# Kernel optimization log

Hardware: AMD Instinct MI355X
Metric: run time of the kernel (lower is better)

## Reference

```python
import jax, jax.numpy as jnp
import numpy as np

B, S, D, P = 8, 2048, 512, 64  # batch, seq, num_embed_hidden, num_attention_project


def setup_inputs() -> dict:
    key = jax.random.key(0)
    ks = jax.random.split(key, 9)
    sd = 1.0 / np.sqrt(D)
    sp = 1.0 / np.sqrt(P)
    return {
        "query": jax.random.normal(ks[0], (B, S, D), dtype=jnp.float32),
        "attention_mask": jnp.ones((B, S), dtype=jnp.float32),
        "Wq": jax.random.uniform(ks[1], (D, P), jnp.float32, -sd, sd),
        "bq": jax.random.uniform(ks[2], (P,), jnp.float32, -sd, sd),
        "Wk": jax.random.uniform(ks[3], (D, P), jnp.float32, -sd, sd),
        "bk": jax.random.uniform(ks[4], (P,), jnp.float32, -sd, sd),
        "Wv": jax.random.uniform(ks[5], (D, P), jnp.float32, -sd, sd),
        "bv": jax.random.uniform(ks[6], (P,), jnp.float32, -sd, sd),
        "Wo": jax.random.uniform(ks[7], (P, D), jnp.float32, -sp, sp),
        "bo": jax.random.uniform(ks[8], (D,), jnp.float32, -sp, sp),
    }


def reference(query, attention_mask, Wq, bq, Wk, bk, Wv, bv, Wo, bo):
    q = jnp.einsum("bsd,dp->bsp", query, Wq) + bq  # [B,S,P]
    k = jnp.einsum("bsd,dp->bsp", query, Wk) + bk
    v = jnp.einsum("bsd,dp->bsp", query, Wv) + bv
    scores = jnp.einsum("bsp,btp->bst", q, k) / jnp.sqrt(jnp.float32(P))  # [B,S,S]
    # Faithful to original: mask broadcast over last axis via unsqueeze(-1) -> masks rows
    scores = scores + (1.0 - attention_mask[:, :, None]) * -10000.0
    weights = jax.nn.softmax(scores, axis=-1)
    weighted = jnp.einsum("bst,btp->bsp", weights, v)
    return jnp.einsum("bsp,pd->bsd", weighted, Wo) + bo
```

## Files before the change

kernel.cpp:

```cpp
#include <hip/hip_runtime.h>
#include <hip/hip_bf16.h>
#include <math.h>

constexpr int B = 8;
constexpr int S = 2048;
constexpr int D = 512;
constexpr int P = 64;
constexpr float SCALE = 0.125f;

typedef short bf16x8 __attribute__((ext_vector_type(8)));
typedef float f32x4 __attribute__((ext_vector_type(4)));
typedef unsigned int u32;

__device__ __forceinline__ unsigned short f2bf(float x) {
  __hip_bfloat16 h = __float2bfloat16(x);
  return __builtin_bit_cast(unsigned short, h);
}
__device__ __forceinline__ float bf2f(unsigned short u) {
  unsigned int v = (unsigned int)u << 16;
  return __builtin_bit_cast(float, v);
}


__global__ __launch_bounds__(256) void prep_w(
    const float* __restrict__ Wq, const float* __restrict__ Wk,
    const float* __restrict__ Wv, const float* __restrict__ Wo,
    unsigned short* __restrict__ Bfrag, unsigned short* __restrict__ Wofrag) {
  const int i = blockIdx.x * 256 + threadIdx.x;
  if (i < 192 * 512) {
    const int d = i / 192;
    const int n = i - d * 192;
    const float* W = (n < 64) ? Wq : (n < 128) ? Wk : Wv;
    const float val = W[d * 64 + (n & 63)];
    const int nt = n >> 4, l15 = n & 15;
    const int k16 = d >> 5, l4 = (d >> 3) & 3, j = d & 7;
    Bfrag[(((nt * 16 + k16) * 4 + l4) * 16 + l15) * 8 + j] = f2bf(val);
  }
  if (i < 64 * 512) {
    const int k = i >> 9;
    const int n = i & 511;
    const float val = Wo[k * 512 + n];
    const int ct = n >> 4, l15 = n & 15;
    const int h = k >> 5, l4 = (k >> 3) & 3, j = k & 7;
    Wofrag[(((ct * 2 + h) * 4 + l4) * 16 + l15) * 8 + j] = f2bf(val);
  }
}

__global__ __launch_bounds__(256, 4) void qkv_mfma(
    const float* __restrict__ query, const unsigned short* __restrict__ Bfrag,
    const float* __restrict__ bq, const float* __restrict__ bk,
    const float* __restrict__ bv, unsigned short* __restrict__ qfrag,
    unsigned short* __restrict__ kfrag, unsigned short* __restrict__ vfrag) {
  __shared__ __align__(16) unsigned short Aq[16 * 512];

  const int tid = threadIdx.x;
  const int w = tid >> 6;
  const int l = tid & 63;
  const int l15 = l & 15;
  const int l4 = l >> 4;
  const int s0 = blockIdx.x * 16;
  const int kb0 = blockIdx.x & 15;

  const float* qsrc = query + (size_t)s0 * D;
#pragma unroll
  for (int step = 0; step < 4; ++step) {
    const int row = step * 4 + w;
    const float* pf = qsrc + row * D + l * 8;
    const float4 x = *(const float4*)pf;
    const float4 y = *(const float4*)(pf + 4);
    bf16x8 u;
    u[0] = (short)f2bf(x.x); u[1] = (short)f2bf(x.y);
    u[2] = (short)f2bf(x.z); u[3] = (short)f2bf(x.w);
    u[4] = (short)f2bf(y.x); u[5] = (short)f2bf(y.y);
    u[6] = (short)f2bf(y.z); u[7] = (short)f2bf(y.w);
    *(bf16x8*)&Aq[row * 512 + ((l ^ (row & 7)) << 3)] = u;
  }
  __syncthreads();

  f32x4 acc[3];
#pragma unroll
  for (int nt = 0; nt < 3; ++nt) acc[nt] = (f32x4){0.f, 0.f, 0.f, 0.f};

#pragma unroll
  for (int kk = 0; kk < 16; ++kk) {
    const int k16 = (kk + kb0) & 15;
    const int aslot = (k16 * 4 + l4) ^ (l15 & 7);
    const bf16x8 af = *(const bf16x8*)&Aq[l15 * 512 + (aslot << 3)];
#pragma unroll
    for (int nt = 0; nt < 3; ++nt) {
      const int ntg = w * 3 + nt;
      const bf16x8 bf =
          *(const bf16x8*)(Bfrag + ((size_t)(ntg * 16 + k16) * 64 + l) * 8);
      acc[nt] = __builtin_amdgcn_mfma_f32_16x16x32_bf16(af, bf, acc[nt], 0, 0,
                                                        0);
    }
  }

  const int b = s0 >> 11;
  const size_t bbase = (size_t)b * (S * P);
#pragma unroll
  for (int nt = 0; nt < 3; ++nt) {
    const int col = w * 48 + nt * 16 + l15;
    const int mat = col >> 6;
    const int p = col & 63;
    const float bb = ((mat == 0) ? bq : (mat == 1) ? bk : bv)[p];
#pragma unroll
    for (int r = 0; r < 4; ++r) {
      const int s = s0 + l4 * 4 + r;
      const int t = s & 2047;
      const float vl = acc[nt][r] + bb;
      if (mat == 2) {
        const int tb = t >> 5, chv = (t >> 3) & 3, jv = t & 7;
        const int pcv = p >> 4, rowv = p & 15;
        vfrag[bbase + (((size_t)(tb * 4 + pcv) * 4 + chv) * 16 + rowv) * 8 +
              jv] = f2bf(vl);
      } else {
        const int tile = t >> 4, rowin = t & 15;
        const int h = p >> 5, chp = (p >> 3) & 3, j = p & 7;
        unsigned short* dst = (mat == 0) ? qfrag : kfrag;
        dst[bbase + (((size_t)(tile * 2 + h) * 4 + chp) * 16 + rowin) * 8 +
            j] = f2bf(mat == 0 ? vl * SCALE : vl);
      }
    }
  }
}

__global__ __launch_bounds__(1024, 4) void attn_fused(
    const unsigned short* __restrict__ qfrag,
    const unsigned short* __restrict__ kfrag,
    const unsigned short* __restrict__ vfrag,
    const unsigned short* __restrict__ Wofrag, const float* __restrict__ bo,
    float* __restrict__ out) {
  __shared__ __align__(16) unsigned char smem[131072];
  __shared__ float l_s[16][32];

  const int tid = threadIdx.x;
  const int w = tid >> 6;
  const int lane = tid & 63;
  const int l15 = lane & 15;
  const int l4 = lane >> 4;
  const int qg = w & 1;
  const int th = w >> 1;

  const int blk = blockIdx.x;
  const int b = blk & 7;
  const int qt = blk >> 3;
  const int s0 = qt * 64;
  const int wst = qt & 3;

  const size_t bbase = (size_t)b * (S * P);
  const unsigned short* qf = qfrag + bbase;
  const unsigned short* kf = kfrag + bbase;
  const unsigned short* vf = vfrag + bbase;

  unsigned short* e_w = (unsigned short*)smem + w * 4096;

  bf16x8 aq[2][2];
#pragma unroll
  for (int st = 0; st < 2; ++st)
#pragma unroll
    for (int h = 0; h < 2; ++h)
      aq[st][h] =
          *(const bf16x8*)(qf +
                           ((size_t)(((s0 >> 4) + qg * 2 + st) * 2 + h) * 64 +
                            lane) *
                               8);

  f32x4 acc[2][4];
#pragma unroll
  for (int st = 0; st < 2; ++st)
#pragma unroll
    for (int pc = 0; pc < 4; ++pc) acc[st][pc] = (f32x4){0.f, 0.f, 0.f, 0.f};
  float lpart[2][4] = {{0.f, 0.f, 0.f, 0.f}, {0.f, 0.f, 0.f, 0.f}};

  for (int win = 0; win < 4; ++win) {
    const int wi = (win + wst) & 3;
    const int t0 = th * 256 + wi * 64;
    unsigned short* e_s = e_w + (win & 1) * 2048;

    bf16x8 bk[4][2];
#pragma unroll
    for (int nt = 0; nt < 4; ++nt)
#pragma unroll
      for (int h = 0; h < 2; ++h)
        bk[nt][h] =
            *(const bf16x8*)(kf +
                             ((size_t)(((t0 >> 4) + nt) * 2 + h) * 64 + lane) *
                                 8);

#pragma unroll
    for (int st = 0; st < 2; ++st) {
      f32x4 sc[4];
#pragma unroll
      for (int nt = 0; nt < 4; ++nt) {
        f32x4 c = (f32x4){0.f, 0.f, 0.f, 0.f};
        c = __builtin_amdgcn_mfma_f32_16x16x32_bf16(aq[st][0], bk[nt][0], c, 0,
                                                    0, 0);
        sc[nt] = __builtin_amdgcn_mfma_f32_16x16x32_bf16(aq[st][1], bk[nt][1],
                                                         c, 0, 0, 0);
      }
#pragma unroll
      for (int nt = 0; nt < 4; ++nt) {
        const int ch = nt * 2 + (l15 >> 3);
#pragma unroll
        for (int r = 0; r < 4; ++r) {
          const int rr = l4 * 4 + r;
          const unsigned short eu = f2bf(__expf(sc[nt][r]));
          lpart[st][r] += bf2f(eu);
          e_s[st * 1024 + rr * 64 + ((ch ^ (rr & 7)) << 3) + (l15 & 7)] = eu;
        }
      }
    }

    bf16x8 bv[4][2];
#pragma unroll
    for (int pc = 0; pc < 4; ++pc)
#pragma unroll
      for (int kk = 0; kk < 2; ++kk)
        bv[pc][kk] =
            *(const bf16x8*)(vf +
                             ((size_t)(((t0 >> 5) + kk) * 4 + pc) * 64 + lane) *
                                 8);

#pragma unroll
    for (int st = 0; st < 2; ++st) {
      bf16x8 ae[2];
#pragma unroll
      for (int kk = 0; kk < 2; ++kk)
        ae[kk] = *(const bf16x8*)&e_s[st * 1024 + l15 * 64 +
                                      (((kk * 4 + l4) ^ (l15 & 7)) << 3)];
#pragma unroll
      for (int pc = 0; pc < 4; ++pc) {
        acc[st][pc] = __builtin_amdgcn_mfma_f32_16x16x32_bf16(
            ae[0], bv[pc][0], acc[st][pc], 0, 0, 0);
        acc[st][pc] = __builtin_amdgcn_mfma_f32_16x16x32_bf16(
            ae[1], bv[pc][1], acc[st][pc], 0, 0, 0);
      }
    }
  }

#pragma unroll
  for (int st = 0; st < 2; ++st)
#pragma unroll
    for (int r = 0; r < 4; ++r) {
      float v = lpart[st][r];
      v += __shfl_xor(v, 1, 64);
      v += __shfl_xor(v, 2, 64);
      v += __shfl_xor(v, 4, 64);
      v += __shfl_xor(v, 8, 64);
      if (l15 == 0) l_s[w][st * 16 + l4 * 4 + r] = v;
    }

  __syncthreads();

  float* pacc = (float*)smem;
  if (th > 0) {
#pragma unroll
    for (int st = 0; st < 2; ++st)
#pragma unroll
      for (int pc = 0; pc < 4; ++pc)
#pragma unroll
        for (int r = 0; r < 4; ++r)
          pacc[((size_t)(qg * 7 + th - 1) * 32 + st * 16 + l4 * 4 + r) * 64 +
               pc * 16 + l15] = acc[st][pc][r];
  }
  __syncthreads();

  unsigned short* wnorm = (unsigned short*)(smem + 114688);
  if (th == 0) {
#pragma unroll
    for (int st = 0; st < 2; ++st) {
      float rl[4];
#pragma unroll
      for (int r = 0; r < 4; ++r) {
        const int row = st * 16 + l4 * 4 + r;
        float ls = 0.f;
#pragma unroll
        for (int t8 = 0; t8 < 8; ++t8) ls += l_s[t8 * 2 + qg][row];
        rl[r] = 1.f / ls;
      }
#pragma unroll
      for (int pc = 0; pc < 4; ++pc)
#pragma unroll
        for (int r = 0; r < 4; ++r) {
          float s = acc[st][pc][r];
#pragma unroll
          for (int j = 0; j < 7; ++j)
            s += pacc[((size_t)(qg * 7 + j) * 32 + st * 16 + l4 * 4 + r) * 64 +
                      pc * 16 + l15];
          wnorm[(qg * 32 + st * 16 + l4 * 4 + r) * 64 + pc * 16 + l15] =
              f2bf(s * rl[r]);
        }
    }
  }
  __syncthreads();

  const int sub = w & 3;
  const int chq = w >> 2;
  const bf16x8 a0 = *(const bf16x8*)&wnorm[(sub * 16 + l15) * 64 + l4 * 8];
  const bf16x8 a1 =
      *(const bf16x8*)&wnorm[(sub * 16 + l15) * 64 + 32 + l4 * 8];
  const size_t orow0 = (size_t)b * S + s0 + sub * 16;
#pragma unroll
  for (int ct = 0; ct < 8; ++ct) {
    const int ctg = chq * 8 + ((ct + (blk & 7)) & 7);
    const bf16x8 b0 =
        *(const bf16x8*)(Wofrag + ((size_t)(ctg * 2 + 0) * 64 + lane) * 8);
    const bf16x8 b1 =
        *(const bf16x8*)(Wofrag + ((size_t)(ctg * 2 + 1) * 64 + lane) * 8);
    f32x4 c = (f32x4){0.f, 0.f, 0.f, 0.f};
    c = __builtin_amdgcn_mfma_f32_16x16x32_bf16(a0, b0, c, 0, 0, 0);
    c = __builtin_amdgcn_mfma_f32_16x16x32_bf16(a1, b1, c, 0, 0, 0);
    const int col = ctg * 16 + l15;
    const float bb = bo[col];
#pragma unroll
    for (int r = 0; r < 4; ++r)
      out[(orow0 + l4 * 4 + r) * D + col] = c[r] + bb;
  }
}

extern "C" void kernel_launch(void* const* d_in, const int* in_sizes, int n_in,
                              void* d_out, int out_size, void* d_ws,
                              size_t ws_size, hipStream_t stream) {
  const float* query = (const float*)d_in[0];
  const float* Wq = (const float*)d_in[2];
  const float* bq = (const float*)d_in[3];
  const float* Wk = (const float*)d_in[4];
  const float* bk = (const float*)d_in[5];
  const float* Wv = (const float*)d_in[6];
  const float* bv = (const float*)d_in[7];
  const float* Wo = (const float*)d_in[8];
  const float* bo = (const float*)d_in[9];
  float* out = (float*)d_out;

  const size_t proj = (size_t)B * S * P;
  unsigned short* qfr = (unsigned short*)d_ws;
  unsigned short* kfr = qfr + proj;
  unsigned short* vfr = kfr + proj;
  unsigned short* Bfrag = vfr + proj;
  unsigned short* Wofrag = Bfrag + 192 * 512;

  prep_w<<<384, 256, 0, stream>>>(Wq, Wk, Wv, Wo, Bfrag, Wofrag);
  qkv_mfma<<<1024, 256, 0, stream>>>(query, Bfrag, bq, bk, bv, qfr, kfr, vfr);
  attn_fused<<<256, 1024, 0, stream>>>(qfr, kfr, vfr, Wofrag, bo, out);
}
```

Before: 139.9 us.

## Stage K/V and weight tiles into LDS via async global-to-LDS loads with double buffering

The QKV projection now processes 64 rows per block with 512 threads. Its weight fragments are staged into double-buffered LDS through global_load_lds, so eight waves share each weight load. The attention kernel handles 128 query rows per block and stages K/V tiles cooperatively into double-buffered LDS, so waves no longer each fetch K/V from global memory. The intent is to cut redundant global/L2 traffic. The cost is half as many blocks (128 attention blocks on a large GPU), which lowers parallelism, plus a barrier per iteration.

```diff
diff --git a/kernel.cpp b/kernel.cpp
--- a/kernel.cpp
+++ b/kernel.cpp
@@ -19,6 +19,13 @@
 __device__ __forceinline__ float bf2f(unsigned short u) {
   unsigned int v = (unsigned int)u << 16;
   return __builtin_bit_cast(float, v);
+}
+
+__device__ __forceinline__ void ld_g2lds16(const unsigned short* g,
+                                           unsigned short* l) {
+  __builtin_amdgcn_global_load_lds(
+      (const __attribute__((address_space(1))) u32*)g,
+      (__attribute__((address_space(3))) u32*)l, 16, 0, 0);
 }
 
 
@@ -46,25 +53,28 @@
   }
 }
 
-__global__ __launch_bounds__(256, 4) void qkv_mfma(
+__global__ __launch_bounds__(512, 2) void qkv_mfma(
     const float* __restrict__ query, const unsigned short* __restrict__ Bfrag,
     const float* __restrict__ bq, const float* __restrict__ bk,
     const float* __restrict__ bv, unsigned short* __restrict__ qfrag,
     unsigned short* __restrict__ kfrag, unsigned short* __restrict__ vfrag) {
-  __shared__ __align__(16) unsigned short Aq[16 * 512];
+  __shared__ __align__(16) unsigned short Aq[64 * 512];
+  __shared__ __align__(16) unsigned short Bb[2][24 * 512];
 
   const int tid = threadIdx.x;
   const int w = tid >> 6;
   const int l = tid & 63;
   const int l15 = l & 15;
   const int l4 = l >> 4;
-  const int s0 = blockIdx.x * 16;
-  const int kb0 = blockIdx.x & 15;
+  const int s0 = blockIdx.x * 64;
+  const int rg = w & 3;
+  const int ch = w >> 2;
+  const int phase = blockIdx.x & 7;
 
   const float* qsrc = query + (size_t)s0 * D;
 #pragma unroll
-  for (int step = 0; step < 4; ++step) {
-    const int row = step * 4 + w;
+  for (int step = 0; step < 8; ++step) {
+    const int row = step * 8 + w;
     const float* pf = qsrc + row * D + l * 8;
     const float4 x = *(const float4*)pf;
     const float4 y = *(const float4*)(pf + 4);
@@ -75,40 +85,58 @@
     u[6] = (short)f2bf(y.z); u[7] = (short)f2bf(y.w);
     *(bf16x8*)&Aq[row * 512 + ((l ^ (row & 7)) << 3)] = u;
   }
+
+#define STAGE_B(kc, buf)                                                      \
+  {                                                                           \
+    _Pragma("unroll") for (int i = 0; i < 3; ++i) {                           \
+      const int cid = w * 3 + i;                                              \
+      const int nt = cid >> 1, kb = cid & 1;                                  \
+      const unsigned short* gp =                                              \
+          Bfrag + (size_t)(nt * 16 + (kc)*2 + kb) * 512 + (size_t)l * 8;      \
+      ld_g2lds16(gp, &Bb[buf][cid * 512]);                                    \
+    }                                                                         \
+  }
+
+  STAGE_B(phase, 0);
   __syncthreads();
 
-  f32x4 acc[3];
-#pragma unroll
-  for (int nt = 0; nt < 3; ++nt) acc[nt] = (f32x4){0.f, 0.f, 0.f, 0.f};
-
-#pragma unroll
-  for (int kk = 0; kk < 16; ++kk) {
-    const int k16 = (kk + kb0) & 15;
-    const int aslot = (k16 * 4 + l4) ^ (l15 & 7);
-    const bf16x8 af = *(const bf16x8*)&Aq[l15 * 512 + (aslot << 3)];
-#pragma unroll
-    for (int nt = 0; nt < 3; ++nt) {
-      const int ntg = w * 3 + nt;
-      const bf16x8 bf =
-          *(const bf16x8*)(Bfrag + ((size_t)(ntg * 16 + k16) * 64 + l) * 8);
-      acc[nt] = __builtin_amdgcn_mfma_f32_16x16x32_bf16(af, bf, acc[nt], 0, 0,
-                                                        0);
-    }
+  f32x4 acc[6];
+#pragma unroll
+  for (int j = 0; j < 6; ++j) acc[j] = (f32x4){0.f, 0.f, 0.f, 0.f};
+
+  for (int it = 0; it < 8; ++it) {
+    const int kc = (it + phase) & 7;
+    if (it < 7) STAGE_B((it + 1 + phase) & 7, (it + 1) & 1);
+    const unsigned short* Bcur = &Bb[it & 1][0];
+#pragma unroll
+    for (int kb = 0; kb < 2; ++kb) {
+      const int row = rg * 16 + l15;
+      const int slot = ((kc * 2 + kb) * 4 + l4) ^ (row & 7);
+      const bf16x8 af = *(const bf16x8*)&Aq[row * 512 + (slot << 3)];
+#pragma unroll
+      for (int j = 0; j < 6; ++j) {
+        const bf16x8 bfr =
+            *(const bf16x8*)&Bcur[((ch * 6 + j) * 2 + kb) * 512 + l * 8];
+        acc[j] =
+            __builtin_amdgcn_mfma_f32_16x16x32_bf16(af, bfr, acc[j], 0, 0, 0);
+      }
+    }
+    __syncthreads();
   }
 
   const int b = s0 >> 11;
   const size_t bbase = (size_t)b * (S * P);
 #pragma unroll
-  for (int nt = 0; nt < 3; ++nt) {
-    const int col = w * 48 + nt * 16 + l15;
+  for (int j = 0; j < 6; ++j) {
+    const int col = ch * 96 + j * 16 + l15;
     const int mat = col >> 6;
     const int p = col & 63;
     const float bb = ((mat == 0) ? bq : (mat == 1) ? bk : bv)[p];
 #pragma unroll
     for (int r = 0; r < 4; ++r) {
-      const int s = s0 + l4 * 4 + r;
+      const int s = s0 + rg * 16 + l4 * 4 + r;
       const int t = s & 2047;
-      const float vl = acc[nt][r] + bb;
+      const float vl = acc[j][r] + bb;
       if (mat == 2) {
         const int tb = t >> 5, chv = (t >> 3) & 3, jv = t & 7;
         const int pcv = p >> 4, rowv = p & 15;
@@ -116,13 +144,14 @@
               jv] = f2bf(vl);
       } else {
         const int tile = t >> 4, rowin = t & 15;
-        const int h = p >> 5, chp = (p >> 3) & 3, j = p & 7;
+        const int h = p >> 5, chp = (p >> 3) & 3, jj = p & 7;
         unsigned short* dst = (mat == 0) ? qfrag : kfrag;
         dst[bbase + (((size_t)(tile * 2 + h) * 4 + chp) * 16 + rowin) * 8 +
-            j] = f2bf(mat == 0 ? vl * SCALE : vl);
-      }
-    }
-  }
+            jj] = f2bf(mat == 0 ? vl * SCALE : vl);
+      }
+    }
+  }
+#undef STAGE_B
 }
 
 __global__ __launch_bounds__(1024, 4) void attn_fused(
@@ -131,7 +160,7 @@
     const unsigned short* __restrict__ vfrag,
     const unsigned short* __restrict__ Wofrag, const float* __restrict__ bo,
     float* __restrict__ out) {
-  __shared__ __align__(16) unsigned char smem[131072];
+  __shared__ __align__(16) unsigned char smem[116736];
   __shared__ float l_s[16][32];
 
   const int tid = threadIdx.x;
@@ -139,21 +168,22 @@
   const int lane = tid & 63;
   const int l15 = lane & 15;
   const int l4 = lane >> 4;
-  const int qg = w & 1;
-  const int th = w >> 1;
+  const int qg = w & 3;
+  const int th = w >> 2;
 
   const int blk = blockIdx.x;
   const int b = blk & 7;
-  const int qt = blk >> 3;
-  const int s0 = qt * 64;
-  const int wst = qt & 3;
+  const int s0 = (blk >> 3) * 128;
+  const int phase = (blk >> 3) & 15;
 
   const size_t bbase = (size_t)b * (S * P);
   const unsigned short* qf = qfrag + bbase;
   const unsigned short* kf = kfrag + bbase;
   const unsigned short* vf = vfrag + bbase;
 
-  unsigned short* e_w = (unsigned short*)smem + w * 4096;
+  unsigned short* kb0 = (unsigned short*)smem;
+  unsigned short* vb0 = (unsigned short*)(smem + 32768);
+  unsigned short* e_w = (unsigned short*)(smem + 65536) + w * 1024;
 
   bf16x8 aq[2][2];
 #pragma unroll
@@ -173,26 +203,43 @@
     for (int pc = 0; pc < 4; ++pc) acc[st][pc] = (f32x4){0.f, 0.f, 0.f, 0.f};
   float lpart[2][4] = {{0.f, 0.f, 0.f, 0.f}, {0.f, 0.f, 0.f, 0.f}};
 
-  for (int win = 0; win < 4; ++win) {
-    const int wi = (win + wst) & 3;
-    const int t0 = th * 256 + wi * 64;
-    unsigned short* e_s = e_w + (win & 1) * 2048;
-
-    bf16x8 bk[4][2];
-#pragma unroll
-    for (int nt = 0; nt < 4; ++nt)
+#define STAGE_KV(wi, buf)                                                     \
+  {                                                                           \
+    const int t0s = (wi)*128;                                                 \
+    const unsigned short* gpk =                                               \
+        kf + ((size_t)((t0s >> 4) + (w >> 1)) * 2 + (w & 1)) * 512 +          \
+        (size_t)lane * 8;                                                     \
+    ld_g2lds16(gpk, kb0 + (buf)*8192 + w * 512);                              \
+    const unsigned short* gpv =                                               \
+        vf + ((size_t)((t0s >> 5) + (w >> 2)) * 4 + (w & 3)) * 512 +          \
+        (size_t)lane * 8;                                                     \
+    ld_g2lds16(gpv, vb0 + (buf)*8192 + w * 512);                              \
+  }
+
+  STAGE_KV(phase, 0);
+  __syncthreads();
+
+  for (int it = 0; it < 16; ++it) {
+    if (it < 15) STAGE_KV((it + 1 + phase) & 15, (it + 1) & 1);
+    const unsigned short* kt = kb0 + (it & 1) * 8192 + th * 2048;
+    const unsigned short* vt = vb0 + (it & 1) * 8192 + th * 2048;
+
+    bf16x8 bk[2][2];
+#pragma unroll
+    for (int nt = 0; nt < 2; ++nt)
 #pragma unroll
       for (int h = 0; h < 2; ++h)
-        bk[nt][h] =
-            *(const bf16x8*)(kf +
-                             ((size_t)(((t0 >> 4) + nt) * 2 + h) * 64 + lane) *
-                                 8);
+        bk[nt][h] = *(const bf16x8*)&kt[nt * 1024 + h * 512 + lane * 8];
+    bf16x8 bv[4];
+#pragma unroll
+    for (int pc = 0; pc < 4; ++pc)
+      bv[pc] = *(const bf16x8*)&vt[pc * 512 + lane * 8];
 
 #pragma unroll
     for (int st = 0; st < 2; ++st) {
-      f32x4 sc[4];
-#pragma unroll
-      for (int nt = 0; nt < 4; ++nt) {
+      f32x4 sc[2];
+#pragma unroll
+      for (int nt = 0; nt < 2; ++nt) {
         f32x4 c = (f32x4){0.f, 0.f, 0.f, 0.f};
         c = __builtin_amdgcn_mfma_f32_16x16x32_bf16(aq[st][0], bk[nt][0], c, 0,
                                                     0, 0);
@@ -200,44 +247,27 @@
                                                          c, 0, 0, 0);
       }
 #pragma unroll
-      for (int nt = 0; nt < 4; ++nt) {
-        const int ch = nt * 2 + (l15 >> 3);
+      for (int nt = 0; nt < 2; ++nt) {
+        const int chl = nt * 2 + (l15 >> 3);
 #pragma unroll
         for (int r = 0; r < 4; ++r) {
           const int rr = l4 * 4 + r;
           const unsigned short eu = f2bf(__expf(sc[nt][r]));
           lpart[st][r] += bf2f(eu);
-          e_s[st * 1024 + rr * 64 + ((ch ^ (rr & 7)) << 3) + (l15 & 7)] = eu;
+          e_w[st * 512 + rr * 32 + ((chl ^ (rr & 3)) << 3) + (l15 & 7)] = eu;
         }
       }
-    }
-
-    bf16x8 bv[4][2];
-#pragma unroll
-    for (int pc = 0; pc < 4; ++pc)
-#pragma unroll
-      for (int kk = 0; kk < 2; ++kk)
-        bv[pc][kk] =
-            *(const bf16x8*)(vf +
-                             ((size_t)(((t0 >> 5) + kk) * 4 + pc) * 64 + lane) *
-                                 8);
-
-#pragma unroll
-    for (int st = 0; st < 2; ++st) {
-      bf16x8 ae[2];
-#pragma unroll
-      for (int kk = 0; kk < 2; ++kk)
-        ae[kk] = *(const bf16x8*)&e_s[st * 1024 + l15 * 64 +
-                                      (((kk * 4 + l4) ^ (l15 & 7)) << 3)];
-#pragma unroll
-      for (int pc = 0; pc < 4; ++pc) {
-        acc[st][pc] = __builtin_amdgcn_mfma_f32_16x16x32_bf16(
-            ae[0], bv[pc][0], acc[st][pc], 0, 0, 0);
-        acc[st][pc] = __builtin_amdgcn_mfma_f32_16x16x32_bf16(
-            ae[1], bv[pc][1], acc[st][pc], 0, 0, 0);
-      }
-    }
-  }
+      const bf16x8 ae =
+          *(const bf16x8*)&e_w[st * 512 + l15 * 32 + ((l4 ^ (l15 & 3)) << 3)];
+#pragma unroll
+      for (int pc = 0; pc < 4; ++pc)
+        acc[st][pc] = __builtin_amdgcn_mfma_f32_16x16x32_bf16(ae, bv[pc],
+                                                              acc[st][pc], 0,
+                                                              0, 0);
+    }
+    __syncthreads();
+  }
+#undef STAGE_KV
 
 #pragma unroll
   for (int st = 0; st < 2; ++st)
@@ -251,8 +281,6 @@
       if (l15 == 0) l_s[w][st * 16 + l4 * 4 + r] = v;
     }
 
-  __syncthreads();
-
   float* pacc = (float*)smem;
   if (th > 0) {
 #pragma unroll
@@ -261,49 +289,46 @@
       for (int pc = 0; pc < 4; ++pc)
 #pragma unroll
         for (int r = 0; r < 4; ++r)
-          pacc[((size_t)(qg * 7 + th - 1) * 32 + st * 16 + l4 * 4 + r) * 64 +
+          pacc[((size_t)(qg * 3 + th - 1) * 32 + st * 16 + l4 * 4 + r) * 64 +
                pc * 16 + l15] = acc[st][pc][r];
   }
   __syncthreads();
 
-  unsigned short* wnorm = (unsigned short*)(smem + 114688);
+  unsigned short* wnorm = (unsigned short*)(smem + 98304);
   if (th == 0) {
 #pragma unroll
     for (int st = 0; st < 2; ++st) {
       float rl[4];
 #pragma unroll
       for (int r = 0; r < 4; ++r) {
-        const int row = st * 16 + l4 * 4 + r;
-        float ls = 0.f;
-#pragma unroll
-        for (int t8 = 0; t8 < 8; ++t8) ls += l_s[t8 * 2 + qg][row];
-        rl[r] = 1.f / ls;
+        const int row32 = st * 16 + l4 * 4 + r;
+        rl[r] = 1.f / (l_s[qg][row32] + l_s[4 + qg][row32] +
+                       l_s[8 + qg][row32] + l_s[12 + qg][row32]);
       }
 #pragma unroll
       for (int pc = 0; pc < 4; ++pc)
 #pragma unroll
         for (int r = 0; r < 4; ++r) {
+          const int row32 = st * 16 + l4 * 4 + r;
           float s = acc[st][pc][r];
 #pragma unroll
-          for (int j = 0; j < 7; ++j)
-            s += pacc[((size_t)(qg * 7 + j) * 32 + st * 16 + l4 * 4 + r) * 64 +
-                      pc * 16 + l15];
-          wnorm[(qg * 32 + st * 16 + l4 * 4 + r) * 64 + pc * 16 + l15] =
-              f2bf(s * rl[r]);
+          for (int j = 0; j < 3; ++j)
+            s += pacc[((size_t)(qg * 3 + j) * 32 + row32) * 64 + pc * 16 +
+                      l15];
+          wnorm[(qg * 32 + row32) * 72 + pc * 16 + l15] = f2bf(s * rl[r]);
         }
     }
   }
   __syncthreads();
 
-  const int sub = w & 3;
-  const int chq = w >> 2;
-  const bf16x8 a0 = *(const bf16x8*)&wnorm[(sub * 16 + l15) * 64 + l4 * 8];
-  const bf16x8 a1 =
-      *(const bf16x8*)&wnorm[(sub * 16 + l15) * 64 + 32 + l4 * 8];
-  const size_t orow0 = (size_t)b * S + s0 + sub * 16;
-#pragma unroll
-  for (int ct = 0; ct < 8; ++ct) {
-    const int ctg = chq * 8 + ((ct + (blk & 7)) & 7);
+  const int rs = w & 7;
+  const int chh = w >> 3;
+  const bf16x8 a0 = *(const bf16x8*)&wnorm[(rs * 16 + l15) * 72 + l4 * 8];
+  const bf16x8 a1 = *(const bf16x8*)&wnorm[(rs * 16 + l15) * 72 + 32 + l4 * 8];
+  const size_t orow0 = (size_t)b * S + s0 + rs * 16;
+#pragma unroll
+  for (int ct = 0; ct < 16; ++ct) {
+    const int ctg = chh * 16 + ((ct + (blk & 15)) & 15);
     const bf16x8 b0 =
         *(const bf16x8*)(Wofrag + ((size_t)(ctg * 2 + 0) * 64 + lane) * 8);
     const bf16x8 b1 =
@@ -341,6 +366,6 @@
   unsigned short* Wofrag = Bfrag + 192 * 512;
 
   prep_w<<<384, 256, 0, stream>>>(Wq, Wk, Wv, Wo, Bfrag, Wofrag);
-  qkv_mfma<<<1024, 256, 0, stream>>>(query, Bfrag, bq, bk, bv, qfr, kfr, vfr);
-  attn_fused<<<256, 1024, 0, stream>>>(qfr, kfr, vfr, Wofrag, bo, out);
-}
+  qkv_mfma<<<256, 512, 0, stream>>>(query, Bfrag, bq, bk, bv, qfr, kfr, vfr);
+  attn_fused<<<128, 1024, 0, stream>>>(qfr, kfr, vfr, Wofrag, bo, out);
+}
```

Result: no change. 140.1 us (+0.2%).
